# Kernel tuning notes

Hardware: AMD Instinct MI355X
Metric: run time of the kernel (lower is better)

Reference implementation:

```python
import jax, jax.numpy as jnp
import numpy as np

B, S, DIM = 2, 2048, 2048
H, KVH, HD = 16, 8, 128
NREP = H // KVH


def _make_freqs(seqlen, head_dim):
    # Rotation-matrix form of RoPE: freqs[s,0,p] = [[cos,-sin],[sin,cos]]
    pos = jnp.arange(seqlen, dtype=jnp.float32)
    inv = 1.0 / (10000.0 ** (jnp.arange(0, head_dim, 2, dtype=jnp.float32) / head_dim))
    ang = pos[:, None] * inv[None, :]                      # (S, HD/2)
    cos, sin = jnp.cos(ang), jnp.sin(ang)
    f = jnp.stack([jnp.stack([cos, -sin], -1),
                   jnp.stack([sin, cos], -1)], -2)          # (S, HD/2, 2, 2)
    return f[:, None]                                       # (S, 1, HD/2, 2, 2)


def setup_inputs() -> dict:
    key = jax.random.key(0)
    k0, k1, k2, k3, k4 = jax.random.split(key, 5)
    x = jax.random.normal(k0, (B, S, DIM), jnp.float32)
    x_mask = jnp.ones((B, S), jnp.bool_)                    # unused by forward
    freqs_cis = _make_freqs(S, HD)
    w_qkv = jax.random.normal(k1, ((H + 2 * KVH) * HD, DIM), jnp.float32) * (DIM ** -0.5)
    w_out = jax.random.normal(k2, (DIM, H * HD), jnp.float32) * ((H * HD) ** -0.5)
    q_norm_w = 1.0 + 0.02 * jax.random.normal(k3, (HD,), jnp.float32)
    k_norm_w = 1.0 + 0.02 * jax.random.normal(k4, (HD,), jnp.float32)
    return {"x": x, "x_mask": x_mask, "freqs_cis": freqs_cis,
            "w_qkv": w_qkv, "w_out": w_out,
            "q_norm_w": q_norm_w, "k_norm_w": k_norm_w}


def _rmsnorm(x, w):
    eps = jnp.asarray(jnp.finfo(x.dtype).eps, x.dtype)
    return x * jax.lax.rsqrt(jnp.mean(x * x, -1, keepdims=True) + eps) * w


def _rope(x, freqs):
    # x: (B,S,h,HD), freqs: (S,1,HD/2,2,2)
    t = x.reshape(*x.shape[:-1], HD // 2, 1, 2)
    out = freqs[..., 0] * t[..., 0] + freqs[..., 1] * t[..., 1]
    return out.reshape(x.shape)


def reference(x, x_mask, freqs_cis, w_qkv, w_out, q_norm_w, k_norm_w):
    b, s, _ = x.shape
    qkv = jnp.einsum('bsd,od->bso', x, w_qkv)
    xq, xk, xv = jnp.split(qkv, [H * HD, (H + KVH) * HD], axis=-1)
    xq = _rope(_rmsnorm(xq.reshape(b, s, H, HD), q_norm_w), freqs_cis)
    xk = _rope(_rmsnorm(xk.reshape(b, s, KVH, HD), k_norm_w), freqs_cis)
    xv = xv.reshape(b, s, KVH, HD)
    # GQA: repeat kv heads (consecutive copies, matching unsqueeze+repeat+flatten)
    xk = jnp.repeat(xk, NREP, axis=2)
    xv = jnp.repeat(xv, NREP, axis=2)
    scale = HD ** -0.5
    scores = jnp.einsum('bqhd,bkhd->bhqk', xq, xk) * scale
    attn = jax.nn.softmax(scores, axis=-1)
    out = jnp.einsum('bhqk,bkhd->bqhd', attn, xv).reshape(b, s, H * HD)
    return jnp.einsum('bso,do->bsd', out, w_out)
```

## Files before the change

kernel.cpp:

```cpp
#include <hip/hip_runtime.h>
#include <hip/hip_bf16.h>
#include <cstdint>

typedef __bf16 bf16_t;
typedef __attribute__((ext_vector_type(8)))  __bf16 bf16x8;
typedef __attribute__((ext_vector_type(4)))  float  f32x4;
typedef __attribute__((ext_vector_type(16))) float  f32x16;

#define AS1 __attribute__((address_space(1)))
#define AS3 __attribute__((address_space(3)))
#define DEV __device__ __forceinline__

#define S_BARRIER() asm volatile("s_barrier" ::: "memory")
#define VMCNT0()    asm volatile("s_waitcnt vmcnt(0)" ::: "memory")
#define SCHED0()    __builtin_amdgcn_sched_barrier(0)

#if __has_builtin(__builtin_amdgcn_exp2f)
#define EXP2(x) __builtin_amdgcn_exp2f(x)
#else
#define EXP2(x) exp2f(x)
#endif

DEV uint32_t pk2bf(float lo, float hi) {
  union { __bf16 h[2]; uint32_t u; } x;
  x.h[0] = (__bf16)lo; x.h[1] = (__bf16)hi; return x.u;
}

__global__ __launch_bounds__(256) void k_cvt(const float* __restrict__ in,
                                             bf16_t* __restrict__ out, int n) {
  int i = (blockIdx.x * 256 + threadIdx.x) * 4;
  if (i + 3 < n) {
    const float4 v = *reinterpret_cast<const float4*>(in + i);
    union { bf16_t h[4]; uint2 u; } o;
    o.h[0] = (bf16_t)v.x; o.h[1] = (bf16_t)v.y;
    o.h[2] = (bf16_t)v.z; o.h[3] = (bf16_t)v.w;
    *reinterpret_cast<uint2*>(out + i) = o.u;
  }
}

#define RD_A_PAIR(dst, base, MF)                                          \
  _Pragma("unroll") for (int j_ = 0; j_ < 2; ++j_)                        \
  _Pragma("unroll") for (int kk_ = 0; kk_ < 2; ++kk_) {                   \
    int p_ = (wm*128 + ((MF)+j_)*16 + c16)*128 + kk_*64 + g*16;           \
    p_ ^= ((p_>>9)&1)<<5;                                                 \
    dst[j_][kk_] = *reinterpret_cast<const bf16x8*>((const char*)(base) + p_); }

#define RD_B_ALL(dst, base)                                               \
  _Pragma("unroll") for (int i_ = 0; i_ < 4; ++i_)                        \
  _Pragma("unroll") for (int kk_ = 0; kk_ < 2; ++kk_) {                   \
    int p_ = (wn*64 + i_*16 + c16)*128 + kk_*64 + g*16;                   \
    p_ ^= ((p_>>9)&1)<<5;                                                 \
    dst[i_][kk_] = *reinterpret_cast<const bf16x8*>((const char*)(base) + p_); }

#define MM_PAIR(aa, MF)                                                   \
  _Pragma("unroll") for (int j_ = 0; j_ < 2; ++j_)                        \
  _Pragma("unroll") for (int i_ = 0; i_ < 4; ++i_)                        \
  _Pragma("unroll") for (int kk_ = 0; kk_ < 2; ++kk_)                     \
    acc[(MF)+j_][i_] = __builtin_amdgcn_mfma_f32_16x16x32_bf16(           \
        aa[j_][kk_], bF[i_][kk_], acc[(MF)+j_][i_], 0, 0, 0);

#define STAGE_A(dstbase, half, tt)                                        \
  _Pragma("unroll") for (int j_ = 0; j_ < 2; ++j_)                        \
    __builtin_amdgcn_global_load_lds(                                     \
        (const AS1 void*)(Ag + srcA[half][j_] + (tt)*64),                 \
        (AS3 void*)((char*)(dstbase) + ((half)*1024 + 512*j_ + wuni)*16), \
        16, 0, 0);

#define STAGE_B(dstbase, half, tt)                                        \
  _Pragma("unroll") for (int j_ = 0; j_ < 2; ++j_)                        \
    __builtin_amdgcn_global_load_lds(                                     \
        (const AS1 void*)(Bg + srcB[half][j_] + (tt)*64),                 \
        (AS3 void*)((char*)(dstbase) + ((half)*1024 + 512*j_ + wuni)*16), \
        16, 0, 0);

__global__ __launch_bounds__(512, 2) void k_gemm256(
    const bf16_t* __restrict__ Ag, const bf16_t* __restrict__ Bg,
    void* __restrict__ Cv, int M, int N, int K, int out_bf16)
{
  extern __shared__ char smemraw[];
  const int tid = threadIdx.x;
  const int w = tid >> 6, l = tid & 63;
  const int wm = w >> 2, wn = w & 3;
  const int c16 = l & 15, g = l >> 4;
  const int wuni = tid & 0x1C0;

  const int nwg = gridDim.x, cpx = nwg >> 3;
  const int bid = blockIdx.x;
  const int L = (bid & 7) * cpx + (bid >> 3);
  const int nbx = N >> 8;
  const int m0 = (L / nbx) * 256, n0 = (L % nbx) * 256;

  int srcA[2][2], srcB[2][2];
#pragma unroll
  for (int half = 0; half < 2; ++half)
#pragma unroll
    for (int j = 0; j < 2; ++j) {
      int ch = half * 1024 + 512 * j + tid;
      int cc = ch ^ (((ch >> 5) & 1) << 1);
      int row = cc >> 3, c8 = (cc & 7) * 8;
      srcA[half][j] = (m0 + row) * K + c8;
      srcB[half][j] = (n0 + row) * K + c8;
    }

  f32x4 acc[8][4] = {};
  bf16x8 aA[2][2], aB[2][2], bF[4][2];

  char* const Ab0 = smemraw;
  char* const Ab1 = smemraw + 32768;
  char* const Bb0 = smemraw + 65536;
  char* const Bb1 = smemraw + 98304;

  const int NT = K >> 6;

  STAGE_A(Ab0, 0, 0); STAGE_A(Ab0, 1, 0);
  STAGE_B(Bb0, 0, 0); STAGE_B(Bb0, 1, 0);
  VMCNT0();
  S_BARRIER();
  RD_A_PAIR(aA, Ab0, 0);
  RD_B_ALL(bF, Bb0);

#pragma unroll 1
  for (int t = 0; t < NT; ++t) {
    char* const Asp = (t & 1) ? Ab1 : Ab0;
    char* const Bsp = (t & 1) ? Bb1 : Bb0;
    char* const Asn = (t & 1) ? Ab0 : Ab1;
    char* const Bsn = (t & 1) ? Bb0 : Bb1;
    const bool more = (t + 1 < NT);

    RD_A_PAIR(aB, Asp, 2);
    if (more) { STAGE_A(Asn, 0, t + 1); STAGE_A(Asn, 1, t + 1); }
    S_BARRIER();
    __builtin_amdgcn_s_setprio(1);
    MM_PAIR(aA, 0);
    __builtin_amdgcn_s_setprio(0); SCHED0();
    S_BARRIER();

    RD_A_PAIR(aA, Asp, 4);
    if (more) { STAGE_B(Bsn, 0, t + 1); STAGE_B(Bsn, 1, t + 1); }
    S_BARRIER();
    __builtin_amdgcn_s_setprio(1);
    MM_PAIR(aB, 2);
    __builtin_amdgcn_s_setprio(0); SCHED0();
    S_BARRIER();

    RD_A_PAIR(aB, Asp, 6);
    S_BARRIER();
    __builtin_amdgcn_s_setprio(1);
    MM_PAIR(aA, 4);
    __builtin_amdgcn_s_setprio(0); SCHED0();
    S_BARRIER();

    if (more) { VMCNT0(); }
    S_BARRIER();
    __builtin_amdgcn_s_setprio(1);
    MM_PAIR(aB, 6);
    __builtin_amdgcn_s_setprio(0); SCHED0();
    if (more) { RD_A_PAIR(aA, Asn, 0); RD_B_ALL(bF, Bsn); }
    S_BARRIER();
  }

#pragma unroll
  for (int mf = 0; mf < 8; ++mf)
#pragma unroll
    for (int nf = 0; nf < 4; ++nf) {
      const int cc = n0 + wn * 64 + nf * 16 + c16;
#pragma unroll
      for (int r = 0; r < 4; ++r) {
        const int rr = m0 + wm * 128 + mf * 16 + g * 4 + r;
        if (out_bf16)
          ((bf16_t*)Cv)[(size_t)rr * N + cc] = (bf16_t)acc[mf][nf][r];
        else
          ((float*)Cv)[(size_t)rr * N + cc] = acc[mf][nf][r];
      }
    }
}

__global__ __launch_bounds__(256, 2) void k_gemm(
    const bf16_t* __restrict__ A, const bf16_t* __restrict__ B,
    void* __restrict__ Cv, int M, int N, int K, int out_bf16)
{
  __shared__ bf16_t Asl[2][128 * 32];
  __shared__ bf16_t Bsl[2][128 * 32];
  const int tid = threadIdx.x;
  const int w = tid >> 6, l = tid & 63;
  const int wr = w >> 1, wc = w & 1;
  const int c16 = l & 15, g = l >> 4;

  const int nwg = gridDim.x, cpx = nwg >> 3;
  const int bid = blockIdx.x;
  const int L = (bid & 7) * cpx + (bid >> 3);
  const int nbx = N >> 7;
  const int m0 = (L / nbx) * 128, n0 = (L % nbx) * 128;

  const bf16_t* Ab = A + (size_t)m0 * K;
  const bf16_t* Bb = B + (size_t)n0 * K;

  f32x4 acc[4][4] = {};

  auto stage = [&](int buf, int kt) {
    const bf16_t* Ag = Ab + kt * 32;
    const bf16_t* Bg = Bb + kt * 32;
#pragma unroll
    for (int i = 0; i < 2; ++i) {
      int ch = tid + 256 * i;
      int row = ch >> 2, kc = ch & 3;
      __builtin_amdgcn_global_load_lds(
          (const AS1 void*)(Ag + (size_t)row * K + kc * 8),
          (AS3 void*)(&Asl[buf][(w * 64 + 256 * i) * 8]), 16, 0, 0);
      __builtin_amdgcn_global_load_lds(
          (const AS1 void*)(Bg + (size_t)row * K + kc * 8),
          (AS3 void*)(&Bsl[buf][(w * 64 + 256 * i) * 8]), 16, 0, 0);
    }
  };

  auto compute = [&](int buf) {
    bf16x8 af[4], bfg[4];
#pragma unroll
    for (int mi = 0; mi < 4; ++mi)
      af[mi] = *reinterpret_cast<const bf16x8*>(
          &Asl[buf][(wr * 64 + mi * 16 + c16) * 32 + g * 8]);
#pragma unroll
    for (int ni = 0; ni < 4; ++ni)
      bfg[ni] = *reinterpret_cast<const bf16x8*>(
          &Bsl[buf][(wc * 64 + ni * 16 + c16) * 32 + g * 8]);
#pragma unroll
    for (int mi = 0; mi < 4; ++mi)
#pragma unroll
      for (int ni = 0; ni < 4; ++ni)
        acc[mi][ni] = __builtin_amdgcn_mfma_f32_16x16x32_bf16(
            af[mi], bfg[ni], acc[mi][ni], 0, 0, 0);
  };

  const int NT = K >> 5;
  stage(0, 0);
  __syncthreads();
  for (int kt = 0; kt < NT - 1; ++kt) {
    stage((kt + 1) & 1, kt + 1);
    compute(kt & 1);
    __syncthreads();
  }
  compute((NT - 1) & 1);

  const int row0 = m0 + wr * 64, col0 = n0 + wc * 64;
#pragma unroll
  for (int mi = 0; mi < 4; ++mi)
#pragma unroll
    for (int ni = 0; ni < 4; ++ni) {
      const int cc = col0 + ni * 16 + c16;
#pragma unroll
      for (int r = 0; r < 4; ++r) {
        const int rr = row0 + mi * 16 + g * 4 + r;
        if (out_bf16)
          ((bf16_t*)Cv)[(size_t)rr * N + cc] = (bf16_t)acc[mi][ni][r];
        else
          ((float*)Cv)[(size_t)rr * N + cc] = acc[mi][ni][r];
      }
    }
}

__global__ __launch_bounds__(256) void k_prep_qk(
    const bf16_t* __restrict__ qkv, const float* __restrict__ freqs,
    const float* __restrict__ qw, const float* __restrict__ kw,
    bf16_t* __restrict__ Qd, bf16_t* __restrict__ Kd)
{
  const int w = threadIdx.x >> 6, l = threadIdx.x & 63;
  const int R = blockIdx.x * 4 + w;
  const int j = R >> 12;
  const int token = R & 4095;
  const int s = token & 2047, b = token >> 11;
  const bool isq = (j < 16);
  const int col0 = isq ? (j << 7) : (2048 + ((j - 16) << 7));

  union { uint32_t u; __bf16 h[2]; } xin;
  xin.u = *reinterpret_cast<const uint32_t*>(qkv + (size_t)token * 4096 + col0 + 2 * l);
  float x0 = (float)xin.h[0], x1 = (float)xin.h[1];
  float ss = x0 * x0 + x1 * x1;
#pragma unroll
  for (int d = 1; d < 64; d <<= 1) ss += __shfl_xor(ss, d, 64);
  const float rn = rsqrtf(ss * (1.0f / 128.0f) + 1.1920929e-7f);
  const float2 wv = *reinterpret_cast<const float2*>((isq ? qw : kw) + 2 * l);
  const float y0 = x0 * rn * wv.x, y1 = x1 * rn * wv.y;
  const float4 f = *reinterpret_cast<const float4*>(freqs + (size_t)s * 256 + l * 4);
  float o0 = f.x * y0 + f.y * y1;
  float o1 = f.z * y0 + f.w * y1;
  if (isq) { o0 *= 0.1275187989014331f; o1 *= 0.1275187989014331f; }
  const uint32_t pk = pk2bf(o0, o1);
  if (isq)
    *reinterpret_cast<uint32_t*>(Qd + ((size_t)(b * 16 + j) * 2048 + s) * 128 + 2 * l) = pk;
  else
    *reinterpret_cast<uint32_t*>(Kd + ((size_t)(b * 8 + (j - 16)) * 2048 + s) * 128 + 2 * l) = pk;
}

__global__ __launch_bounds__(256) void k_prep_v(const bf16_t* __restrict__ qkv,
                                                bf16_t* __restrict__ Vt)
{
  __shared__ bf16_t vt[64][136];
  const int tid = threadIdx.x;
  const int bid = blockIdx.x;
  const int st = bid & 31, kh = (bid >> 5) & 7, b = bid >> 8;
  const int s0 = st * 64;
#pragma unroll
  for (int i = 0; i < 4; ++i) {
    int ch = tid + 256 * i;
    int srow = ch >> 4, d8 = ch & 15;
    bf16x8 v = *reinterpret_cast<const bf16x8*>(
        qkv + (size_t)(b * 2048 + s0 + srow) * 4096 + 3072 + kh * 128 + d8 * 8);
    *reinterpret_cast<bf16x8*>(&vt[srow][d8 * 8]) = v;
  }
  __syncthreads();
  const int d = tid >> 1, sc = tid & 1;
  bf16_t* dst = Vt + ((size_t)(b * 8 + kh) * 128 + d) * 2048 + s0 + 32 * sc;
#pragma unroll
  for (int grp = 0; grp < 4; ++grp) {
    uint32_t pk[4];
#pragma unroll
    for (int q = 0; q < 4; ++q) {
      int jj = 32 * sc + grp * 8 + q * 2;
      union { __bf16 h[2]; uint32_t u; } e;
      e.h[0] = vt[jj][d]; e.h[1] = vt[jj + 1][d];
      pk[q] = e.u;
    }
    uint4 o; o.x = pk[0]; o.y = pk[1]; o.z = pk[2]; o.w = pk[3];
    *reinterpret_cast<uint4*>(dst + grp * 8) = o;
  }
}

__global__ __launch_bounds__(256, 2) void k_attn(
    const bf16_t* __restrict__ Qd, const bf16_t* __restrict__ Kd,
    const bf16_t* __restrict__ Vt, bf16_t* __restrict__ O)
{
  __shared__ bf16_t kbuf[2][64 * 128];
  __shared__ bf16_t vbuf[2][128 * 64];
  const int tid = threadIdx.x;
  const int w = tid >> 6, l = tid & 63;
  const int c = l & 31, h2 = l >> 5;
  const int bid = blockIdx.x;
  const int qt = bid & 15, h = (bid >> 4) & 15, b = bid >> 8;
  const int kvh = h >> 1;
  const bf16_t* Qg = Qd + ((size_t)(b * 16 + h) * 2048 + qt * 128 + w * 32) * 128;
  const bf16_t* Kg = Kd + ((size_t)(b * 8 + kvh) * 2048) * 128;
  const bf16_t* Vg = Vt + ((size_t)(b * 8 + kvh) * 128) * 2048;

  bf16x8 qf[8];
#pragma unroll
  for (int s = 0; s < 8; ++s)
    qf[s] = *reinterpret_cast<const bf16x8*>(Qg + (size_t)c * 128 + s * 16 + h2 * 8);

  f32x16 oacc[4] = {};
  float l0 = 0.f, l1 = 0.f, l2 = 0.f, l3 = 0.f;

  auto stage = [&](int buf, int kt) {
#pragma unroll
    for (int i = 0; i < 4; ++i) {
      int ch = tid + 256 * i;
      {
        int key = ch >> 4, d16 = ch & 15;
        int soff = key * 256 + ((d16 * 16) ^ ((key & 7) << 4));
        __builtin_amdgcn_global_load_lds(
            (const AS1 void*)((const char*)Kg + (size_t)kt * 64 * 256 + soff),
            (AS3 void*)((char*)&kbuf[buf][0] + (w * 64 + 256 * i) * 16), 16, 0, 0);
      }
      {
        int d = ch >> 3, k8 = (ch & 7) ^ (d & 7);
        __builtin_amdgcn_global_load_lds(
            (const AS1 void*)(Vg + (size_t)d * 2048 + kt * 64 + k8 * 8),
            (AS3 void*)((char*)&vbuf[buf][0] + (w * 64 + 256 * i) * 16), 16, 0, 0);
      }
    }
  };

  auto compute = [&](int buf) {
    f32x16 sacc[2] = {};
    const char* kb = (const char*)&kbuf[buf][0];
    __builtin_amdgcn_s_setprio(1);
#pragma unroll
    for (int m = 0; m < 2; ++m)
#pragma unroll
      for (int s = 0; s < 8; ++s) {
        int byte = (m * 32 + c) * 256 + ((s * 32 + h2 * 16) ^ ((c & 7) << 4));
        bf16x8 kf = *reinterpret_cast<const bf16x8*>(kb + byte);
        sacc[m] = __builtin_amdgcn_mfma_f32_32x32x16_bf16(kf, qf[s], sacc[m], 0, 0, 0);
      }
    __builtin_amdgcn_s_setprio(0);

#pragma unroll
    for (int m = 0; m < 2; ++m)
#pragma unroll
      for (int r = 0; r < 16; r += 4) {
        float p0 = EXP2(sacc[m][r + 0]);
        float p1 = EXP2(sacc[m][r + 1]);
        float p2 = EXP2(sacc[m][r + 2]);
        float p3 = EXP2(sacc[m][r + 3]);
        sacc[m][r + 0] = p0; sacc[m][r + 1] = p1;
        sacc[m][r + 2] = p2; sacc[m][r + 3] = p3;
        l0 += p0; l1 += p1; l2 += p2; l3 += p3;
      }

    const char* vb = (const char*)&vbuf[buf][0];
#pragma unroll
    for (int t = 0; t < 4; ++t) {
      const int m = t >> 1, q2i = t & 1;
      uint32_t u0 = pk2bf(sacc[m][8 * q2i + 0], sacc[m][8 * q2i + 1]);
      uint32_t u1 = pk2bf(sacc[m][8 * q2i + 2], sacc[m][8 * q2i + 3]);
      uint32_t u2 = pk2bf(sacc[m][8 * q2i + 4], sacc[m][8 * q2i + 5]);
      uint32_t u3 = pk2bf(sacc[m][8 * q2i + 6], sacc[m][8 * q2i + 7]);
      auto r02 = __builtin_amdgcn_permlane32_swap((int)u0, (int)u2, false, false);
      auto r13 = __builtin_amdgcn_permlane32_swap((int)u1, (int)u3, false, false);
      union { uint32_t u[4]; bf16x8 v; } pb;
      pb.u[0] = (uint32_t)r02[0]; pb.u[1] = (uint32_t)r13[0];
      pb.u[2] = (uint32_t)r02[1]; pb.u[3] = (uint32_t)r13[1];
      __builtin_amdgcn_s_setprio(1);
#pragma unroll
      for (int df = 0; df < 4; ++df) {
        int byte = (df * 32 + c) * 128 + ((t * 32 + h2 * 16) ^ ((c & 7) << 4));
        bf16x8 vf = *reinterpret_cast<const bf16x8*>(vb + byte);
        oacc[df] = __builtin_amdgcn_mfma_f32_32x32x16_bf16(vf, pb.v, oacc[df], 0, 0, 0);
      }
      __builtin_amdgcn_s_setprio(0);
    }
  };

  stage(0, 0);
  __syncthreads();
  for (int kt = 0; kt < 31; ++kt) {
    stage((kt + 1) & 1, kt + 1);
    compute(kt & 1);
    __syncthreads();
  }
  compute(1);

  float lrun = (l0 + l1) + (l2 + l3);
  lrun += __shfl_xor(lrun, 32, 64);
  const float inv = 1.0f / lrun;
  bf16_t* Og = O + ((size_t)(b * 2048 + qt * 128 + w * 32 + c) * 2048) + h * 128;
#pragma unroll
  for (int df = 0; df < 4; ++df)
#pragma unroll
    for (int rg = 0; rg < 4; ++rg) {
      uint32_t w0 = pk2bf(oacc[df][rg * 4 + 0] * inv, oacc[df][rg * 4 + 1] * inv);
      uint32_t w1 = pk2bf(oacc[df][rg * 4 + 2] * inv, oacc[df][rg * 4 + 3] * inv);
      uint2 ww; ww.x = w0; ww.y = w1;
      *reinterpret_cast<uint2*>(Og + df * 32 + 8 * rg + 4 * h2) = ww;
    }
}

extern "C" void kernel_launch(void* const* d_in, const int* in_sizes, int n_in,
                              void* d_out, int out_size, void* d_ws, size_t ws_size,
                              hipStream_t stream)
{
  const float* x     = (const float*)d_in[0];
  const float* freqs = (const float*)d_in[2];
  const float* wqkv  = (const float*)d_in[3];
  const float* wout  = (const float*)d_in[4];
  const float* qw    = (const float*)d_in[5];
  const float* kw    = (const float*)d_in[6];
  float* out = (float*)d_out;

  bf16_t* Xb   = (bf16_t*)d_ws;
  bf16_t* Wqb  = Xb  + 8388608;
  bf16_t* Wob  = Wqb + 8388608;
  bf16_t* qkvb = Wob + 4194304;
  bf16_t* Qdp  = qkvb + 16777216;
  bf16_t* Kdp  = Qdp + 8388608;
  bf16_t* Vtp  = Kdp + 4194304;
  bf16_t* Ob   = qkvb;

  (void)hipFuncSetAttribute((const void*)k_gemm256,
                            hipFuncAttributeMaxDynamicSharedMemorySize, 131072);

  k_cvt<<<8192, 256, 0, stream>>>(x, Xb, 8388608);
  k_cvt<<<8192, 256, 0, stream>>>(wqkv, Wqb, 8388608);
  k_cvt<<<4096, 256, 0, stream>>>(wout, Wob, 4194304);
  k_gemm256<<<256, 512, 131072, stream>>>(Xb, Wqb, qkvb, 4096, 4096, 2048, 1);
  k_prep_qk<<<24576, 256, 0, stream>>>(qkvb, freqs, qw, kw, Qdp, Kdp);
  k_prep_v<<<512, 256, 0, stream>>>(qkvb, Vtp);
  k_attn<<<512, 256, 0, stream>>>(Qdp, Kdp, Vtp, Ob);
  k_gemm<<<512, 256, 0, stream>>>(Ob, Wob, out, 4096, 2048, 2048, 0);
}
```

Baseline: 241.4 us.

## Load attention K/V fragments directly from global and merge fp32-to-bf16 conversions

The attention kernel no longer stages K and V tiles into double-buffered LDS with async global-to-LDS loads and barriers. Each wave now reads its K and V fragments straight from global memory into registers right before the MFMAs, which removes LDS traffic and synchronisation. The cost is redundant global/L2 reads across the four waves that share a KV tile, and load latency is exposed without the prefetch pipeline. Separately, the three fp32-to-bf16 conversion launches are merged into one kernel that relies on the workspace buffers being contiguous.

```diff
diff --git a/kernel.cpp b/kernel.cpp
--- a/kernel.cpp
+++ b/kernel.cpp
@@ -26,16 +26,21 @@
   x.h[0] = (__bf16)lo; x.h[1] = (__bf16)hi; return x.u;
 }
 
-__global__ __launch_bounds__(256) void k_cvt(const float* __restrict__ in,
-                                             bf16_t* __restrict__ out, int n) {
-  int i = (blockIdx.x * 256 + threadIdx.x) * 4;
-  if (i + 3 < n) {
-    const float4 v = *reinterpret_cast<const float4*>(in + i);
-    union { bf16_t h[4]; uint2 u; } o;
-    o.h[0] = (bf16_t)v.x; o.h[1] = (bf16_t)v.y;
-    o.h[2] = (bf16_t)v.z; o.h[3] = (bf16_t)v.w;
-    *reinterpret_cast<uint2*>(out + i) = o.u;
-  }
+__global__ __launch_bounds__(256) void k_cvt3(const float* __restrict__ s0,
+                                              const float* __restrict__ s1,
+                                              const float* __restrict__ s2,
+                                              bf16_t* __restrict__ dst) {
+  long i = (long)(blockIdx.x * 256 + threadIdx.x) * 4;
+  const float* src;
+  long off;
+  if (i < 8388608)        { src = s0; off = i; }
+  else if (i < 16777216)  { src = s1; off = i - 8388608; }
+  else                    { src = s2; off = i - 16777216; }
+  const float4 v = *reinterpret_cast<const float4*>(src + off);
+  union { bf16_t h[4]; uint2 u; } o;
+  o.h[0] = (bf16_t)v.x; o.h[1] = (bf16_t)v.y;
+  o.h[2] = (bf16_t)v.z; o.h[3] = (bf16_t)v.w;
+  *reinterpret_cast<uint2*>(dst + i) = o.u;
 }
 
 #define RD_A_PAIR(dst, base, MF)                                          \
@@ -329,8 +334,6 @@
     const bf16_t* __restrict__ Qd, const bf16_t* __restrict__ Kd,
     const bf16_t* __restrict__ Vt, bf16_t* __restrict__ O)
 {
-  __shared__ bf16_t kbuf[2][64 * 128];
-  __shared__ bf16_t vbuf[2][128 * 64];
   const int tid = threadIdx.x;
   const int w = tid >> 6, l = tid & 63;
   const int c = l & 31, h2 = l >> 5;
@@ -349,39 +352,25 @@
   f32x16 oacc[4] = {};
   float l0 = 0.f, l1 = 0.f, l2 = 0.f, l3 = 0.f;
 
-  auto stage = [&](int buf, int kt) {
-#pragma unroll
-    for (int i = 0; i < 4; ++i) {
-      int ch = tid + 256 * i;
-      {
-        int key = ch >> 4, d16 = ch & 15;
-        int soff = key * 256 + ((d16 * 16) ^ ((key & 7) << 4));
-        __builtin_amdgcn_global_load_lds(
-            (const AS1 void*)((const char*)Kg + (size_t)kt * 64 * 256 + soff),
-            (AS3 void*)((char*)&kbuf[buf][0] + (w * 64 + 256 * i) * 16), 16, 0, 0);
-      }
-      {
-        int d = ch >> 3, k8 = (ch & 7) ^ (d & 7);
-        __builtin_amdgcn_global_load_lds(
-            (const AS1 void*)(Vg + (size_t)d * 2048 + kt * 64 + k8 * 8),
-            (AS3 void*)((char*)&vbuf[buf][0] + (w * 64 + 256 * i) * 16), 16, 0, 0);
-      }
-    }
-  };
-
-  auto compute = [&](int buf) {
+#pragma unroll 1
+  for (int kt = 0; kt < 32; ++kt) {
+    const bf16_t* Kt = Kg + (size_t)kt * 64 * 128;
+    const bf16_t* Vt2 = Vg + kt * 64;
+
     f32x16 sacc[2] = {};
-    const char* kb = (const char*)&kbuf[buf][0];
-    __builtin_amdgcn_s_setprio(1);
-#pragma unroll
-    for (int m = 0; m < 2; ++m)
-#pragma unroll
-      for (int s = 0; s < 8; ++s) {
-        int byte = (m * 32 + c) * 256 + ((s * 32 + h2 * 16) ^ ((c & 7) << 4));
-        bf16x8 kf = *reinterpret_cast<const bf16x8*>(kb + byte);
-        sacc[m] = __builtin_amdgcn_mfma_f32_32x32x16_bf16(kf, qf[s], sacc[m], 0, 0, 0);
-      }
-    __builtin_amdgcn_s_setprio(0);
+#pragma unroll
+    for (int m = 0; m < 2; ++m) {
+      bf16x8 kf[8];
+#pragma unroll
+      for (int s = 0; s < 8; ++s)
+        kf[s] = *reinterpret_cast<const bf16x8*>(
+            Kt + (size_t)(m * 32 + c) * 128 + s * 16 + h2 * 8);
+      __builtin_amdgcn_s_setprio(1);
+#pragma unroll
+      for (int s = 0; s < 8; ++s)
+        sacc[m] = __builtin_amdgcn_mfma_f32_32x32x16_bf16(kf[s], qf[s], sacc[m], 0, 0, 0);
+      __builtin_amdgcn_s_setprio(0);
+    }
 
 #pragma unroll
     for (int m = 0; m < 2; ++m)
@@ -396,7 +385,6 @@
         l0 += p0; l1 += p1; l2 += p2; l3 += p3;
       }
 
-    const char* vb = (const char*)&vbuf[buf][0];
 #pragma unroll
     for (int t = 0; t < 4; ++t) {
       const int m = t >> 1, q2i = t & 1;
@@ -409,25 +397,18 @@
       union { uint32_t u[4]; bf16x8 v; } pb;
       pb.u[0] = (uint32_t)r02[0]; pb.u[1] = (uint32_t)r13[0];
       pb.u[2] = (uint32_t)r02[1]; pb.u[3] = (uint32_t)r13[1];
+      bf16x8 vf[4];
+#pragma unroll
+      for (int df = 0; df < 4; ++df)
+        vf[df] = *reinterpret_cast<const bf16x8*>(
+            Vt2 + (size_t)(df * 32 + c) * 2048 + t * 16 + h2 * 8);
       __builtin_amdgcn_s_setprio(1);
 #pragma unroll
-      for (int df = 0; df < 4; ++df) {
-        int byte = (df * 32 + c) * 128 + ((t * 32 + h2 * 16) ^ ((c & 7) << 4));
-        bf16x8 vf = *reinterpret_cast<const bf16x8*>(vb + byte);
-        oacc[df] = __builtin_amdgcn_mfma_f32_32x32x16_bf16(vf, pb.v, oacc[df], 0, 0, 0);
-      }
+      for (int df = 0; df < 4; ++df)
+        oacc[df] = __builtin_amdgcn_mfma_f32_32x32x16_bf16(vf[df], pb.v, oacc[df], 0, 0, 0);
       __builtin_amdgcn_s_setprio(0);
     }
-  };
-
-  stage(0, 0);
-  __syncthreads();
-  for (int kt = 0; kt < 31; ++kt) {
-    stage((kt + 1) & 1, kt + 1);
-    compute(kt & 1);
-    __syncthreads();
   }
-  compute(1);
 
   float lrun = (l0 + l1) + (l2 + l3);
   lrun += __shfl_xor(lrun, 32, 64);
@@ -468,9 +449,7 @@
   (void)hipFuncSetAttribute((const void*)k_gemm256,
                             hipFuncAttributeMaxDynamicSharedMemorySize, 131072);
 
-  k_cvt<<<8192, 256, 0, stream>>>(x, Xb, 8388608);
-  k_cvt<<<8192, 256, 0, stream>>>(wqkv, Wqb, 8388608);
-  k_cvt<<<4096, 256, 0, stream>>>(wout, Wob, 4194304);
+  k_cvt3<<<20480, 256, 0, stream>>>(x, wqkv, wout, Xb);
   k_gemm256<<<256, 512, 131072, stream>>>(Xb, Wqb, qkvb, 4096, 4096, 2048, 1);
   k_prep_qk<<<24576, 256, 0, stream>>>(qkvb, freqs, qw, kw, Qdp, Kdp);
   k_prep_v<<<512, 256, 0, stream>>>(qkvb, Vtp);
```

New measurement: 387.5 us. 60.6% more time.
